# Performance work log

Measured on AMD Instinct MI355X. Metric: run time of the kernel, lower is better.

Reference implementation:

```python
import jax, jax.numpy as jnp
import numpy as np

B, N, H, V = 2048, 16, 512, 780  # trees, nodes per tree, hidden size, vocab size


def _topology():
    """Build one random tree, replicate across B trees, and precompute the
    BFS level schedule on the non-backtracking line graph (as DGL's
    level_order: reversed(edges_back) = up edges leaves-first, then
    edges = down edges root-first)."""
    rng = np.random.default_rng(0)
    parent = np.zeros(N, dtype=np.int64)
    for i in range(1, N):
        parent[i] = rng.integers(0, i)
    depth = np.zeros(N, dtype=np.int64)
    for i in range(1, N):
        depth[i] = depth[parent[i]] + 1
    Epc = 2 * (N - 1)  # directed edges per tree
    src = np.zeros(Epc, dtype=np.int64)
    dst = np.zeros(Epc, dtype=np.int64)
    for i in range(1, N):
        src[2 * (i - 1)] = parent[i]; dst[2 * (i - 1)] = i          # down edge
        src[2 * (i - 1) + 1] = i;     dst[2 * (i - 1) + 1] = parent[i]  # up edge
    # line-graph predecessors of edge e=(u->v): edges f=(w->u) with w != v
    preds = [[f for f in range(Epc) if dst[f] == src[e] and src[f] != dst[e]]
             for e in range(Epc)]
    P = max(1, max(len(p) for p in preds))
    preds_pad = np.full((Epc, P), -1, dtype=np.int64)
    for e, p in enumerate(preds):
        preds_pad[e, :len(p)] = p
    D = int(depth.max())
    levels = []
    for d in range(D, 0, -1):   # upward pass, deepest level first
        levels.append([2 * (i - 1) + 1 for i in range(1, N) if depth[i] == d])
    for d in range(1, D + 1):   # downward pass, root first
        levels.append([2 * (i - 1) for i in range(1, N) if depth[i] == d])
    E = B * Epc                 # index E is the zero dummy row
    offs = np.arange(B, dtype=np.int64) * Epc
    preds_full = np.where(preds_pad[None] >= 0,
                          preds_pad[None] + offs[:, None, None], E)
    preds_full = preds_full.reshape(E, P)
    preds_full = np.concatenate(
        [preds_full, np.full((1, P), E, dtype=np.int64)], axis=0)  # [E+1, P]
    Mmax = max(len(lv) for lv in levels) * B
    lv_arr = np.full((len(levels), Mmax), E, dtype=np.int64)
    for l, lv in enumerate(levels):
        ids = (np.asarray(lv, np.int64)[None] + offs[:, None]).reshape(-1)
        lv_arr[l, :ids.size] = ids
    edge_src = (src[None] + np.arange(B, dtype=np.int64)[:, None] * N).reshape(-1)
    root_children = [2 * (i - 1) + 1 for i in range(1, N) if parent[i] == 0]
    root_in = np.asarray(root_children, np.int64)[None] + offs[:, None]  # [B, R]
    root_nodes = np.arange(B, dtype=np.int64) * N
    return edge_src, preds_full, lv_arr, root_in, root_nodes


def setup_inputs() -> dict:
    key = jax.random.key(0)
    ks = jax.random.split(key, 11)
    edge_src, preds, levels, root_in, root_nodes = _topology()
    s1 = 1.0 / np.sqrt(H)
    s2 = 1.0 / np.sqrt(2 * H)
    return {
        "wid": jax.random.randint(ks[0], (B * N,), 0, V),
        "edge_src": jnp.asarray(edge_src),
        "preds": jnp.asarray(preds),
        "levels": jnp.asarray(levels),
        "root_in": jnp.asarray(root_in),
        "root_nodes": jnp.asarray(root_nodes),
        "emb": jax.random.normal(ks[1], (V, H), jnp.float32),
        "w_r": jax.random.normal(ks[2], (H, H), jnp.float32) * s1,
        "ur_w": jax.random.normal(ks[3], (H, H), jnp.float32) * s1,
        "ur_b": jax.random.normal(ks[4], (H,), jnp.float32) * s1,
        "wz_w": jax.random.normal(ks[5], (2 * H, H), jnp.float32) * s2,
        "wz_b": jax.random.normal(ks[6], (H,), jnp.float32) * s2,
        "wh_w": jax.random.normal(ks[7], (2 * H, H), jnp.float32) * s2,
        "wh_b": jax.random.normal(ks[8], (H,), jnp.float32) * s2,
        "wo_w": jax.random.normal(ks[9], (2 * H, H), jnp.float32) * s2,
        "wo_b": jax.random.normal(ks[10], (H,), jnp.float32) * s2,
    }


def reference(wid, edge_src, preds, levels, root_in, root_nodes,
              emb, w_r, ur_w, ur_b, wz_w, wz_b, wh_w, wh_b, wo_w, wo_b):
    E = edge_src.shape[0]
    Hd = emb.shape[1]
    x = emb[wid]                                           # [B*N, H]
    zero = jnp.zeros((1, Hd), x.dtype)
    sx_all = x[edge_src]                                   # src_x per edge
    src_x = jnp.concatenate([sx_all, zero], axis=0)        # [E+1, H], row E = 0
    src_x_r = jnp.concatenate([sx_all @ w_r, zero], axis=0)  # W_r (no bias)
    h = jnp.zeros((E + 1, Hd), x.dtype)
    for l in range(levels.shape[0]):                       # static BFS levels
        idx = levels[l]                                    # [M], padded with E
        p = preds[idx]                                     # [M, P]
        h_nei = h[p]                                       # [M, P, H]
        sum_h = h_nei.sum(axis=1)
        # GRUMessage: r = sigmoid(dst.src_x_r + U_r(src.h)); m = r * src.h
        r = jax.nn.sigmoid(src_x_r[idx][:, None, :] + h_nei @ ur_w + ur_b)
        sum_g = (r * h_nei).sum(axis=1)
        sx = src_x[idx]
        # GRUUpdate
        z = jax.nn.sigmoid(jnp.concatenate([sx, sum_h], axis=-1) @ wz_w + wz_b)
        pre_h = jnp.tanh(jnp.concatenate([sx, sum_g], axis=-1) @ wh_w + wh_b)
        h = h.at[idx].set((1.0 - z) * sum_h + z * pre_h)
        h = h.at[E].set(0.0)                               # keep dummy row zero
    h_edges = h[:E]                                        # edata['h']
    h_root = h[root_in].sum(axis=1)                        # pull into roots
    x_root = x[root_nodes]
    root_vec = jax.nn.relu(
        jnp.concatenate([x_root, h_root], axis=-1) @ wo_w + wo_b)
    return h_edges, root_vec
```

## Files before the change

kernel.cpp:

```cpp
#include <hip/hip_runtime.h>
#include <hip/hip_bf16.h>
#include <cstddef>

#define HD 512

typedef short s8v __attribute__((ext_vector_type(8)));
typedef short s4v __attribute__((ext_vector_type(4)));
typedef float fx4 __attribute__((ext_vector_type(4)));

#define MFMA(a, b, c) __builtin_amdgcn_mfma_f32_16x16x32_bf16((a), (b), (c), 0, 0, 0)

__device__ __forceinline__ unsigned short f2bf(float f) {
  unsigned int u = __float_as_uint(f);
  unsigned int r = (u + 0x7fffu + ((u >> 16) & 1u)) >> 16;
  return (unsigned short)r;
}
__device__ __forceinline__ float bf2f(unsigned short u) {
  return __uint_as_float(((unsigned int)u) << 16);
}

__device__ __forceinline__ size_t swz_off(int k, int n, int KT) {
  int kt = k >> 5, kr = k & 31;
  int nt = n >> 4, nr = n & 15;
  int lane = ((kr >> 3) << 4) | nr;
  int i = kr & 7;
  return ((((size_t)nt * KT + kt) * 64 + lane) << 3) + i;
}

__global__ void pack_kernel(const float* w_r, const float* ur, const float* wz, const float* wh,
                            const float* wo,
                            unsigned short* W1, unsigned short* WZB, unsigned short* WHB,
                            unsigned short* WUR, unsigned short* WO) {
  int idx = blockIdx.x * blockDim.x + threadIdx.x;
  int stride = gridDim.x * blockDim.x;
  for (int t = idx; t < 512 * 1536; t += stride) {
    int k = t / 1536, n = t - k * 1536;
    float v;
    if (n < 512) v = w_r[k * 512 + n];
    else if (n < 1024) v = wz[k * 512 + (n - 512)];
    else v = wh[k * 512 + (n - 1024)];
    W1[swz_off(k, n, 16)] = f2bf(v);
  }
  for (int t = idx; t < 512 * 512; t += stride) {
    int k = t >> 9, n = t & 511;
    size_t o = swz_off(k, n, 16);
    WZB[o] = f2bf(wz[(512 + k) * 512 + n]);
    WHB[o] = f2bf(wh[(512 + k) * 512 + n]);
    WUR[o] = f2bf(ur[k * 512 + n]);
  }
  for (int t = idx; t < 1024 * 512; t += stride) {
    int k = t >> 9, n = t & 511;
    WO[swz_off(k, n, 32)] = f2bf(wo[k * 512 + n]);
  }
}

__global__ void embed_kernel(const int* wid, const float* emb, unsigned short* x_bf, int BN) {
  int idx = blockIdx.x * blockDim.x + threadIdx.x;
  int stride = gridDim.x * blockDim.x;
  int total = BN * (HD / 8);
  for (int t = idx; t < total; t += stride) {
    int nrow = t >> 6;
    int c8 = (t & 63) << 3;
    int w = wid[nrow];
    const float4* s = (const float4*)(emb + (size_t)w * HD + c8);
    float4 v0 = s[0], v1 = s[1];
    s8v o;
    o[0] = (short)f2bf(v0.x); o[1] = (short)f2bf(v0.y);
    o[2] = (short)f2bf(v0.z); o[3] = (short)f2bf(v0.w);
    o[4] = (short)f2bf(v1.x); o[5] = (short)f2bf(v1.y);
    o[6] = (short)f2bf(v1.z); o[7] = (short)f2bf(v1.w);
    *(s8v*)&x_bf[(size_t)nrow * HD + c8] = o;
  }
}

__global__ void schedule_kernel(const int* preds, int E, int Epc, int P, int* sched) {
  __shared__ int rnd[64];
  int t = threadIdx.x;
  rnd[t] = -1;
  __syncthreads();
  for (int it = 0; it <= Epc; ++it) {
    int newv = -1;
    if (t < Epc && rnd[t] < 0) {
      int mx = 0;
      bool ready = true;
      for (int q = 0; q < P; ++q) {
        int pe = preds[t * P + q];
        if (pe < E) {
          int rp = rnd[pe];
          if (rp < 0) ready = false;
          else if (rp + 1 > mx) mx = rp + 1;
        }
      }
      if (ready) newv = mx;
    }
    __syncthreads();
    if (newv >= 0) rnd[t] = newv;
    __syncthreads();
  }
  if (t == 0) {
    int R = 0;
    for (int e = 0; e < Epc; ++e) if (rnd[e] + 1 > R) R = rnd[e] + 1;
    if (R > 31) R = 31;
    sched[0] = R;
    for (int r = 0; r < 31; ++r) {
      int c = 0;
      if (r < R) {
        for (int e = 0; e < Epc; ++e) if (rnd[e] == r) { sched[33 + r * 32 + c] = e; ++c; }
      }
      sched[1 + r] = c;
    }
  }
}

__global__ __launch_bounds__(512, 4) void gemm_pre_kernel(const unsigned short* x_bf,
                                                          const unsigned short* W1,
                                                          unsigned short* XP, int BN) {
  __shared__ unsigned short lA[2][128 * 72];
  const int nM = BN >> 7;
  const int slab = blockIdx.x / nM;
  const int mt = blockIdx.x - slab * nM;
  const int tid = threadIdx.x, lane = tid & 63, w = tid >> 6;
  const int wm = w & 1, wn = w >> 1;
  const int m0 = mt << 7;
  const int srow = tid >> 2, sc0 = (tid & 3) << 4;
  const int k8 = (lane >> 4) << 3;
  fx4 ac[16];
#pragma unroll
  for (int i = 0; i < 16; i++) { ac[i][0]=0.f; ac[i][1]=0.f; ac[i][2]=0.f; ac[i][3]=0.f; }
  const unsigned short* aptr = x_bf + (size_t)(m0 + srow) * 512 + sc0;
  s8v r0, r1;
  {
    r0 = *(const s8v*)aptr;
    r1 = *(const s8v*)(aptr + 8);
    *(s8v*)&lA[0][srow * 72 + sc0]     = r0;
    *(s8v*)&lA[0][srow * 72 + sc0 + 8] = r1;
    r0 = *(const s8v*)(aptr + 64);
    r1 = *(const s8v*)(aptr + 72);
  }
  for (int ks = 0; ks < 8; ++ks) {
    const int cur = ks & 1;
    __syncthreads();
    if (ks < 7) {
      *(s8v*)&lA[cur ^ 1][srow * 72 + sc0]     = r0;
      *(s8v*)&lA[cur ^ 1][srow * 72 + sc0 + 8] = r1;
    }
    if (ks < 6) {
      const unsigned short* g = aptr + ((ks + 2) << 6);
      r0 = *(const s8v*)g;
      r1 = *(const s8v*)(g + 8);
    }
#pragma unroll
    for (int sub = 0; sub < 2; ++sub) {
      const int kt = (ks << 1) + sub;
      s8v a[4];
#pragma unroll
      for (int mi = 0; mi < 4; ++mi)
        a[mi] = *(const s8v*)&lA[cur][((wm << 6) + (mi << 4) + (lane & 15)) * 72 + (sub << 5) + k8];
#pragma unroll
      for (int ni = 0; ni < 4; ++ni) {
        const int ntile = (slab << 4) + (wn << 2) + ni;
        const s8v b = *(const s8v*)(W1 + ((((size_t)ntile << 4) + kt) * 64 + lane) * 8);
#pragma unroll
        for (int mi = 0; mi < 4; ++mi) ac[mi * 4 + ni] = MFMA(a[mi], b, ac[mi * 4 + ni]);
      }
    }
  }
#pragma unroll
  for (int mi = 0; mi < 4; ++mi) {
#pragma unroll
    for (int q = 0; q < 4; ++q) {
      const int row = (wm << 6) + (mi << 4) + ((lane >> 4) << 2) + q;
#pragma unroll
      for (int ni = 0; ni < 4; ++ni) {
        const int col = (slab << 8) + (wn << 6) + (ni << 4) + (lane & 15);
        XP[(size_t)(m0 + row) * 1536 + col] = f2bf(ac[mi * 4 + ni][q]);
      }
    }
  }
}

struct AP {
  const int* sched;
  const int* preds;
  const int* edge_src;
  const float* ur_b;
  const unsigned short* XP;
  const unsigned short* u_bf_c;
  const unsigned short* hE_c;
  unsigned short* A2h;
  unsigned short* A2g;
  int* eIdx;
  int* srcIdx;
  int B, Epc, P, E;
};

__global__ __launch_bounds__(256) void gatherA_kernel(AP p, int r) {
  const int cnt = p.sched[1 + r];
  if (cnt == 0) return;
  const int M = cnt * p.B;
  const int* lst = p.sched + 33 + r * 32;
  const int lane = threadIdx.x & 63;
  const int waveId = blockIdx.x * 4 + (threadIdx.x >> 6);
  const int totalWaves = gridDim.x * 4;
  for (int m = waveId; m < M; m += totalWaves) {
    const int b = m / cnt;
    const int j = m - b * cnt;
    const int e = b * p.Epc + lst[j];
    const int src = p.edge_src[e];
    if (lane == 0) { p.eIdx[m] = e; p.srcIdx[m] = src; }
    const int c0 = lane << 3;
    const s8v xr8 = *(const s8v*)&p.XP[(size_t)src * 1536 + c0];
    float xb[8], ub[8], sh[8], sg[8];
#pragma unroll
    for (int i = 0; i < 8; i++) {
      xb[i] = bf2f((unsigned short)xr8[i]);
      ub[i] = p.ur_b[c0 + i];
      sh[i] = 0.f; sg[i] = 0.f;
    }
    for (int t = 0; t < p.P; ++t) {
      const int pe = p.preds[(size_t)e * p.P + t];
      if (pe >= p.E) continue;
      const s8v h8 = *(const s8v*)&p.hE_c[(size_t)pe * 512 + c0];
      const s8v u8 = *(const s8v*)&p.u_bf_c[(size_t)pe * 512 + c0];
#pragma unroll
      for (int i = 0; i < 8; i++) {
        const float hv = bf2f((unsigned short)h8[i]);
        const float rr = 1.f / (1.f + __expf(-(xb[i] + bf2f((unsigned short)u8[i]) + ub[i])));
        sh[i] += hv;
        sg[i] += rr * hv;
      }
    }
    s8v shb, sgb;
#pragma unroll
    for (int i = 0; i < 8; i++) { shb[i] = (short)f2bf(sh[i]); sgb[i] = (short)f2bf(sg[i]); }
    *(s8v*)&p.A2h[(size_t)m * 512 + c0] = shb;
    *(s8v*)&p.A2g[(size_t)m * 512 + c0] = sgb;
  }
}

struct BP {
  const int* sched;
  const float* wz_b;
  const float* wh_b;
  const unsigned short* XP;
  const unsigned short* A2h;
  const unsigned short* A2g;
  const unsigned short* WZB;
  const unsigned short* WHB;
  const int* eIdx;
  const int* srcIdx;
  unsigned short* hE;
  int B;
};

__global__ __launch_bounds__(256, 4) void gemmB_kernel(BP p, int r) {
  const int cnt = p.sched[1 + r];
  if (cnt == 0) return;
  const int M = cnt * p.B;
  const int nT = (M >> 5) << 1;
  const int qq = nT >> 3;
  __shared__ unsigned short lZ[2][32 * 72];
  __shared__ unsigned short lH[2][32 * 72];
  __shared__ int eL[32];
  __shared__ int sL[32];
  const int tid = threadIdx.x, lane = tid & 63, w = tid >> 6;
  const int srow = tid >> 3, sc = (tid & 7) << 3;
  const int k8 = (lane >> 4) << 3;

  for (int t0 = blockIdx.x; t0 < nT; t0 += gridDim.x) {
    const int t = (t0 & 7) * qq + (t0 >> 3);
    const int mt = t >> 1, nb = t & 1;
    const int m0 = mt << 5, n0 = nb << 8;
    if (tid < 32) { eL[tid] = p.eIdx[m0 + tid]; sL[tid] = p.srcIdx[m0 + tid]; }
    fx4 aZ[8], aH[8];
#pragma unroll
    for (int i = 0; i < 8; i++) {
      aZ[i][0]=0.f; aZ[i][1]=0.f; aZ[i][2]=0.f; aZ[i][3]=0.f;
      aH[i][0]=0.f; aH[i][1]=0.f; aH[i][2]=0.f; aH[i][3]=0.f;
    }
    const size_t rbase = (size_t)(m0 + srow) * 512 + sc;
    s8v nh, ng;
    {
      *(s8v*)&lZ[0][srow * 72 + sc] = *(const s8v*)&p.A2h[rbase];
      *(s8v*)&lH[0][srow * 72 + sc] = *(const s8v*)&p.A2g[rbase];
      nh = *(const s8v*)&p.A2h[rbase + 64];
      ng = *(const s8v*)&p.A2g[rbase + 64];
    }
    for (int ks = 0; ks < 8; ++ks) {
      const int cur = ks & 1;
      __syncthreads();
      if (ks < 7) {
        *(s8v*)&lZ[cur ^ 1][srow * 72 + sc] = nh;
        *(s8v*)&lH[cur ^ 1][srow * 72 + sc] = ng;
      }
      if (ks < 6) {
        nh = *(const s8v*)&p.A2h[rbase + ((ks + 2) << 6)];
        ng = *(const s8v*)&p.A2g[rbase + ((ks + 2) << 6)];
      }
#pragma unroll
      for (int sub = 0; sub < 2; ++sub) {
        const int kt = (ks << 1) + sub;
        s8v az[2], ah[2];
#pragma unroll
        for (int mi = 0; mi < 2; ++mi) {
          const int ao = ((mi << 4) + (lane & 15)) * 72 + (sub << 5) + k8;
          az[mi] = *(const s8v*)&lZ[cur][ao];
          ah[mi] = *(const s8v*)&lH[cur][ao];
        }
#pragma unroll
        for (int ni = 0; ni < 4; ++ni) {
          const int ntile = (n0 >> 4) + (w << 2) + ni;
          const size_t boff = ((((size_t)ntile << 4) + kt) * 64 + lane) << 3;
          const s8v bz = *(const s8v*)(p.WZB + boff);
          const s8v bh = *(const s8v*)(p.WHB + boff);
#pragma unroll
          for (int mi = 0; mi < 2; ++mi) {
            aZ[mi * 4 + ni] = MFMA(az[mi], bz, aZ[mi * 4 + ni]);
            aH[mi * 4 + ni] = MFMA(ah[mi], bh, aH[mi * 4 + ni]);
          }
        }
      }
    }
#pragma unroll
    for (int mi = 0; mi < 2; ++mi) {
#pragma unroll
      for (int q4 = 0; q4 < 4; ++q4) {
        const int row = (mi << 4) + ((lane >> 4) << 2) + q4;
        const int e = eL[row];
        const int src = sL[row];
#pragma unroll
        for (int ni = 0; ni < 4; ++ni) {
          const int col = n0 + (w << 6) + (ni << 4) + (lane & 15);
          float zpre = aZ[mi * 4 + ni][q4] + bf2f(p.XP[(size_t)src * 1536 + 512 + col]) + p.wz_b[col];
          float hpre = aH[mi * 4 + ni][q4] + bf2f(p.XP[(size_t)src * 1536 + 1024 + col]) + p.wh_b[col];
          float zz = 1.f / (1.f + __expf(-zpre));
          float e2 = __expf(2.f * hpre);
          float th = 1.f - 2.f / (e2 + 1.f);
          float sumh = bf2f(p.A2h[(size_t)(m0 + row) * 512 + col]);
          float hn = (1.f - zz) * sumh + zz * th;
          p.hE[(size_t)e * 512 + col] = f2bf(hn);
        }
      }
    }
    __syncthreads();
  }
}

struct CP {
  const int* sched;
  const unsigned short* hE;
  const unsigned short* WUR;
  const int* eIdx;
  unsigned short* u_bf;
  int B;
};

__global__ __launch_bounds__(256, 4) void gemmC_kernel(CP p, int r) {
  const int cnt = p.sched[1 + r];
  if (cnt == 0) return;
  const int M = cnt * p.B;
  const int nT = (M >> 5) << 1;
  const int qq = nT >> 3;
  __shared__ unsigned short lA[2][32 * 72];
  __shared__ int eL[32];
  const int tid = threadIdx.x, lane = tid & 63, w = tid >> 6;
  const int srow = tid >> 3, sc = (tid & 7) << 3;
  const int k8 = (lane >> 4) << 3;

  for (int t0 = blockIdx.x; t0 < nT; t0 += gridDim.x) {
    const int t = (t0 & 7) * qq + (t0 >> 3);
    const int mt = t >> 1, nb = t & 1;
    const int m0 = mt << 5, n0 = nb << 8;
    if (tid < 32) eL[tid] = p.eIdx[m0 + tid];
    __syncthreads();
    fx4 ac[8];
#pragma unroll
    for (int i = 0; i < 8; i++) { ac[i][0]=0.f; ac[i][1]=0.f; ac[i][2]=0.f; ac[i][3]=0.f; }
    const unsigned short* gbase = p.hE + (size_t)eL[srow] * 512 + sc;
    s8v ra;
    {
      *(s8v*)&lA[0][srow * 72 + sc] = *(const s8v*)gbase;
      ra = *(const s8v*)(gbase + 64);
    }
    for (int ks = 0; ks < 8; ++ks) {
      const int cur = ks & 1;
      __syncthreads();
      if (ks < 7) {
        *(s8v*)&lA[cur ^ 1][srow * 72 + sc] = ra;
      }
      if (ks < 6) {
        ra = *(const s8v*)(gbase + ((ks + 2) << 6));
      }
#pragma unroll
      for (int sub = 0; sub < 2; ++sub) {
        const int kt = (ks << 1) + sub;
        s8v a[2];
#pragma unroll
        for (int mi = 0; mi < 2; ++mi)
          a[mi] = *(const s8v*)&lA[cur][((mi << 4) + (lane & 15)) * 72 + (sub << 5) + k8];
#pragma unroll
        for (int ni = 0; ni < 4; ++ni) {
          const int ntile = (n0 >> 4) + (w << 2) + ni;
          const size_t boff = ((((size_t)ntile << 4) + kt) * 64 + lane) << 3;
          const s8v bu = *(const s8v*)(p.WUR + boff);
#pragma unroll
          for (int mi = 0; mi < 2; ++mi) ac[mi * 4 + ni] = MFMA(a[mi], bu, ac[mi * 4 + ni]);
        }
      }
    }
#pragma unroll
    for (int mi = 0; mi < 2; ++mi) {
#pragma unroll
      for (int q4 = 0; q4 < 4; ++q4) {
        const int row = (mi << 4) + ((lane >> 4) << 2) + q4;
        const int e = eL[row];
#pragma unroll
        for (int ni = 0; ni < 4; ++ni) {
          const int col = n0 + (w << 6) + (ni << 4) + (lane & 15);
          p.u_bf[(size_t)e * 512 + col] = f2bf(ac[mi * 4 + ni][q4]);
        }
      }
    }
    __syncthreads();
  }
}

__global__ void cvt_kernel(const unsigned short* hE, float* h, int total8) {
  int idx = blockIdx.x * blockDim.x + threadIdx.x;
  int stride = gridDim.x * blockDim.x;
  for (int t = idx; t < total8; t += stride) {
    const s8v v = *(const s8v*)&hE[(size_t)t * 8];
    float4 f0 = make_float4(bf2f((unsigned short)v[0]), bf2f((unsigned short)v[1]),
                            bf2f((unsigned short)v[2]), bf2f((unsigned short)v[3]));
    float4 f1 = make_float4(bf2f((unsigned short)v[4]), bf2f((unsigned short)v[5]),
                            bf2f((unsigned short)v[6]), bf2f((unsigned short)v[7]));
    *(float4*)&h[(size_t)t * 8] = f0;
    *(float4*)&h[(size_t)t * 8 + 4] = f1;
  }
}

__global__ void root_gather_kernel(const int* root_nodes, const int* root_in,
                                   const unsigned short* x_bf, const unsigned short* hE,
                                   unsigned short* Aroot, int B, int R0) {
  int lane = threadIdx.x & 63;
  int waveId = blockIdx.x * (blockDim.x >> 6) + (threadIdx.x >> 6);
  int totalWaves = gridDim.x * (blockDim.x >> 6);
  for (int b = waveId; b < B; b += totalWaves) {
    int c0 = lane << 3;
    int nd = root_nodes[b];
    *(s8v*)&Aroot[(size_t)b * 1024 + c0] = *(const s8v*)&x_bf[(size_t)nd * HD + c0];
    float s[8];
#pragma unroll
    for (int i = 0; i < 8; i++) s[i] = 0.f;
    for (int t = 0; t < R0; ++t) {
      int e = root_in[b * R0 + t];
      const s8v h8 = *(const s8v*)&hE[(size_t)e * 512 + c0];
#pragma unroll
      for (int i = 0; i < 8; i++) s[i] += bf2f((unsigned short)h8[i]);
    }
    s8v sb;
#pragma unroll
    for (int i = 0; i < 8; i++) sb[i] = (short)f2bf(s[i]);
    *(s8v*)&Aroot[(size_t)b * 1024 + 512 + c0] = sb;
  }
}

__global__ __launch_bounds__(256, 4) void gemm_root_kernel(const unsigned short* Aroot,
                                                           const unsigned short* WO,
                                                           const float* wo_b, float* out, int B) {
  const int nT = (B >> 5) << 1;
  __shared__ unsigned short lA[2][32 * 72];
  const int tid = threadIdx.x, lane = tid & 63, w = tid >> 6;
  const int srow = tid >> 3, sc = (tid & 7) << 3;
  const int k8 = (lane >> 4) << 3;

  for (int t = blockIdx.x; t < nT; t += gridDim.x) {
    const int mt = t >> 1, nb = t & 1;
    const int m0 = mt << 5, n0 = nb << 8;
    fx4 ac[8];
#pragma unroll
    for (int i = 0; i < 8; i++) { ac[i][0]=0.f; ac[i][1]=0.f; ac[i][2]=0.f; ac[i][3]=0.f; }
    const unsigned short* gbase = Aroot + (size_t)(m0 + srow) * 1024 + sc;
    s8v ra;
    {
      *(s8v*)&lA[0][srow * 72 + sc] = *(const s8v*)gbase;
      ra = *(const s8v*)(gbase + 64);
    }
    for (int ks = 0; ks < 16; ++ks) {
      const int cur = ks & 1;
      __syncthreads();
      if (ks < 15) {
        *(s8v*)&lA[cur ^ 1][srow * 72 + sc] = ra;
      }
      if (ks < 14) {
        ra = *(const s8v*)(gbase + ((ks + 2) << 6));
      }
#pragma unroll
      for (int sub = 0; sub < 2; ++sub) {
        const int kt = (ks << 1) + sub;
        s8v a[2];
#pragma unroll
        for (int mi = 0; mi < 2; ++mi)
          a[mi] = *(const s8v*)&lA[cur][((mi << 4) + (lane & 15)) * 72 + (sub << 5) + k8];
#pragma unroll
        for (int ni = 0; ni < 4; ++ni) {
          const int ntile = (n0 >> 4) + (w << 2) + ni;
          const size_t boff = (((size_t)ntile * 32 + kt) * 64 + lane) << 3;
          const s8v b = *(const s8v*)(WO + boff);
#pragma unroll
          for (int mi = 0; mi < 2; ++mi) ac[mi * 4 + ni] = MFMA(a[mi], b, ac[mi * 4 + ni]);
        }
      }
    }
#pragma unroll
    for (int mi = 0; mi < 2; ++mi) {
#pragma unroll
      for (int q4 = 0; q4 < 4; ++q4) {
        const int row = (mi << 4) + ((lane >> 4) << 2) + q4;
        const int m = m0 + row;
#pragma unroll
        for (int ni = 0; ni < 4; ++ni) {
          const int col = n0 + (w << 6) + (ni << 4) + (lane & 15);
          float v = ac[mi * 4 + ni][q4] + wo_b[col];
          out[(size_t)m * HD + col] = v > 0.f ? v : 0.f;
        }
      }
    }
    __syncthreads();
  }
}

extern "C" void kernel_launch(void* const* d_in, const int* in_sizes, int n_in,
                              void* d_out, int out_size, void* d_ws, size_t ws_size,
                              hipStream_t stream) {
  const int* wid = (const int*)d_in[0];
  const int* edge_src = (const int*)d_in[1];
  const int* preds = (const int*)d_in[2];
  const int* root_in = (const int*)d_in[4];
  const int* root_nodes = (const int*)d_in[5];
  const float* emb = (const float*)d_in[6];
  const float* w_r = (const float*)d_in[7];
  const float* ur_w = (const float*)d_in[8];
  const float* ur_b = (const float*)d_in[9];
  const float* wz_w = (const float*)d_in[10];
  const float* wz_b = (const float*)d_in[11];
  const float* wh_w = (const float*)d_in[12];
  const float* wh_b = (const float*)d_in[13];
  const float* wo_w = (const float*)d_in[14];
  const float* wo_b = (const float*)d_in[15];

  const int BN = in_sizes[0];
  const int E = in_sizes[1];
  const int Bt = in_sizes[5];
  const int Epc = E / Bt;
  const int P = in_sizes[2] / (E + 1);
  const int R0 = in_sizes[4] / Bt;

  float* h = (float*)d_out;

  char* wp = (char*)d_ws;
  auto alloc = [&](size_t bytes) {
    char* r = wp;
    wp += (bytes + 255) & ~(size_t)255;
    return r;
  };
  unsigned short* x_bf = (unsigned short*)alloc((size_t)BN * 512 * 2);
  unsigned short* XP = (unsigned short*)alloc((size_t)BN * 1536 * 2);
  unsigned short* u_bf = (unsigned short*)alloc((size_t)E * 512 * 2);
  unsigned short* hE = (unsigned short*)alloc((size_t)E * 512 * 2);
  unsigned short* A2h = (unsigned short*)alloc((size_t)E * 512 * 2);
  unsigned short* A2g = (unsigned short*)alloc((size_t)E * 512 * 2);
  int* eIdx = (int*)alloc((size_t)E * 4);
  int* srcIdx = (int*)alloc((size_t)E * 4);
  unsigned short* W1 = (unsigned short*)alloc((size_t)512 * 1536 * 2);
  unsigned short* WZB = (unsigned short*)alloc((size_t)512 * 512 * 2);
  unsigned short* WHB = (unsigned short*)alloc((size_t)512 * 512 * 2);
  unsigned short* WUR = (unsigned short*)alloc((size_t)512 * 512 * 2);
  unsigned short* WO = (unsigned short*)alloc((size_t)1024 * 512 * 2);
  unsigned short* Aroot = (unsigned short*)alloc((size_t)Bt * 1024 * 2);
  int* sched = (int*)alloc(8192);

  hipLaunchKernelGGL(pack_kernel, dim3(512), dim3(256), 0, stream,
                     w_r, ur_w, wz_w, wh_w, wo_w, W1, WZB, WHB, WUR, WO);
  hipLaunchKernelGGL(embed_kernel, dim3(1024), dim3(256), 0, stream, wid, emb, x_bf, BN);
  hipLaunchKernelGGL(schedule_kernel, dim3(1), dim3(64), 0, stream, preds, E, Epc, P, sched);
  hipLaunchKernelGGL(gemm_pre_kernel, dim3((BN / 128) * 6), dim3(512), 0, stream,
                     x_bf, W1, XP, BN);

  AP ap;
  ap.sched = sched; ap.preds = preds; ap.edge_src = edge_src;
  ap.ur_b = ur_b; ap.XP = XP; ap.u_bf_c = u_bf; ap.hE_c = hE;
  ap.A2h = A2h; ap.A2g = A2g; ap.eIdx = eIdx; ap.srcIdx = srcIdx;
  ap.B = Bt; ap.Epc = Epc; ap.P = P; ap.E = E;

  BP bp;
  bp.sched = sched; bp.wz_b = wz_b; bp.wh_b = wh_b;
  bp.XP = XP; bp.A2h = A2h; bp.A2g = A2g;
  bp.WZB = WZB; bp.WHB = WHB;
  bp.eIdx = eIdx; bp.srcIdx = srcIdx;
  bp.hE = hE; bp.B = Bt;

  CP cp;
  cp.sched = sched; cp.hE = hE; cp.WUR = WUR;
  cp.eIdx = eIdx; cp.u_bf = u_bf; cp.B = Bt;

  for (int r = 0; r < Epc && r < 31; ++r) {
    const int g = (r < 16) ? 1024 : 128;
    hipLaunchKernelGGL(gatherA_kernel, dim3(g), dim3(256), 0, stream, ap, r);
    hipLaunchKernelGGL(gemmB_kernel, dim3(g), dim3(256), 0, stream, bp, r);
    hipLaunchKernelGGL(gemmC_kernel, dim3(g), dim3(256), 0, stream, cp, r);
  }

  hipLaunchKernelGGL(cvt_kernel, dim3(2048), dim3(256), 0, stream, hE, h, E * 64);
  hipLaunchKernelGGL(root_gather_kernel, dim3(512), dim3(256), 0, stream,
                     root_nodes, root_in, x_bf, hE, Aroot, Bt, R0);
  hipLaunchKernelGGL(gemm_root_kernel, dim3((Bt / 32) * 2), dim3(256), 0, stream,
                     Aroot, WO, wo_b, h + (size_t)E * 512, Bt);
}
```

Baseline: 944.7 us.

## Interleave h and U_r(h) rows into one buffer, chunk gather loop, shrink late grids

```diff
diff --git a/kernel.cpp b/kernel.cpp
--- a/kernel.cpp
+++ b/kernel.cpp
@@ -185,8 +185,7 @@
   const int* edge_src;
   const float* ur_b;
   const unsigned short* XP;
-  const unsigned short* u_bf_c;
-  const unsigned short* hE_c;
+  const unsigned short* hu_c;
   unsigned short* A2h;
   unsigned short* A2g;
   int* eIdx;
@@ -202,7 +201,10 @@
   const int lane = threadIdx.x & 63;
   const int waveId = blockIdx.x * 4 + (threadIdx.x >> 6);
   const int totalWaves = gridDim.x * 4;
-  for (int m = waveId; m < M; m += totalWaves) {
+  const int chunk = (M + totalWaves - 1) / totalWaves;
+  const int mBeg = waveId * chunk;
+  const int mEnd = (mBeg + chunk < M) ? (mBeg + chunk) : M;
+  for (int m = mBeg; m < mEnd; ++m) {
     const int b = m / cnt;
     const int j = m - b * cnt;
     const int e = b * p.Epc + lst[j];
@@ -220,8 +222,9 @@
     for (int t = 0; t < p.P; ++t) {
       const int pe = p.preds[(size_t)e * p.P + t];
       if (pe >= p.E) continue;
-      const s8v h8 = *(const s8v*)&p.hE_c[(size_t)pe * 512 + c0];
-      const s8v u8 = *(const s8v*)&p.u_bf_c[(size_t)pe * 512 + c0];
+      const unsigned short* hurow = p.hu_c + (size_t)pe * 1024;
+      const s8v h8 = *(const s8v*)&hurow[c0];
+      const s8v u8 = *(const s8v*)&hurow[512 + c0];
 #pragma unroll
       for (int i = 0; i < 8; i++) {
         const float hv = bf2f((unsigned short)h8[i]);
@@ -249,7 +252,7 @@
   const unsigned short* WHB;
   const int* eIdx;
   const int* srcIdx;
-  unsigned short* hE;
+  unsigned short* hu;
   int B;
 };
 
@@ -338,7 +341,7 @@
           float th = 1.f - 2.f / (e2 + 1.f);
           float sumh = bf2f(p.A2h[(size_t)(m0 + row) * 512 + col]);
           float hn = (1.f - zz) * sumh + zz * th;
-          p.hE[(size_t)e * 512 + col] = f2bf(hn);
+          p.hu[(size_t)e * 1024 + col] = f2bf(hn);
         }
       }
     }
@@ -348,10 +351,9 @@
 
 struct CP {
   const int* sched;
-  const unsigned short* hE;
   const unsigned short* WUR;
   const int* eIdx;
-  unsigned short* u_bf;
+  unsigned short* hu;
   int B;
 };
 
@@ -376,7 +378,7 @@
     fx4 ac[8];
 #pragma unroll
     for (int i = 0; i < 8; i++) { ac[i][0]=0.f; ac[i][1]=0.f; ac[i][2]=0.f; ac[i][3]=0.f; }
-    const unsigned short* gbase = p.hE + (size_t)eL[srow] * 512 + sc;
+    const unsigned short* gbase = p.hu + (size_t)eL[srow] * 1024 + sc;
     s8v ra;
     {
       *(s8v*)&lA[0][srow * 72 + sc] = *(const s8v*)gbase;
@@ -417,7 +419,7 @@
 #pragma unroll
         for (int ni = 0; ni < 4; ++ni) {
           const int col = n0 + (w << 6) + (ni << 4) + (lane & 15);
-          p.u_bf[(size_t)e * 512 + col] = f2bf(ac[mi * 4 + ni][q4]);
+          p.hu[(size_t)e * 1024 + 512 + col] = f2bf(ac[mi * 4 + ni][q4]);
         }
       }
     }
@@ -425,22 +427,24 @@
   }
 }
 
-__global__ void cvt_kernel(const unsigned short* hE, float* h, int total8) {
+__global__ void cvt_kernel(const unsigned short* hu, float* h, int total8) {
   int idx = blockIdx.x * blockDim.x + threadIdx.x;
   int stride = gridDim.x * blockDim.x;
   for (int t = idx; t < total8; t += stride) {
-    const s8v v = *(const s8v*)&hE[(size_t)t * 8];
+    const int row = t >> 6;
+    const int c8 = (t & 63) << 3;
+    const s8v v = *(const s8v*)&hu[(size_t)row * 1024 + c8];
     float4 f0 = make_float4(bf2f((unsigned short)v[0]), bf2f((unsigned short)v[1]),
                             bf2f((unsigned short)v[2]), bf2f((unsigned short)v[3]));
     float4 f1 = make_float4(bf2f((unsigned short)v[4]), bf2f((unsigned short)v[5]),
                             bf2f((unsigned short)v[6]), bf2f((unsigned short)v[7]));
-    *(float4*)&h[(size_t)t * 8] = f0;
-    *(float4*)&h[(size_t)t * 8 + 4] = f1;
+    *(float4*)&h[(size_t)row * 512 + c8] = f0;
+    *(float4*)&h[(size_t)row * 512 + c8 + 4] = f1;
   }
 }
 
 __global__ void root_gather_kernel(const int* root_nodes, const int* root_in,
-                                   const unsigned short* x_bf, const unsigned short* hE,
+                                   const unsigned short* x_bf, const unsigned short* hu,
                                    unsigned short* Aroot, int B, int R0) {
   int lane = threadIdx.x & 63;
   int waveId = blockIdx.x * (blockDim.x >> 6) + (threadIdx.x >> 6);
@@ -454,7 +458,7 @@
     for (int i = 0; i < 8; i++) s[i] = 0.f;
     for (int t = 0; t < R0; ++t) {
       int e = root_in[b * R0 + t];
-      const s8v h8 = *(const s8v*)&hE[(size_t)e * 512 + c0];
+      const s8v h8 = *(const s8v*)&hu[(size_t)e * 1024 + c0];
 #pragma unroll
       for (int i = 0; i < 8; i++) s[i] += bf2f((unsigned short)h8[i]);
     }
@@ -566,8 +570,7 @@
   };
   unsigned short* x_bf = (unsigned short*)alloc((size_t)BN * 512 * 2);
   unsigned short* XP = (unsigned short*)alloc((size_t)BN * 1536 * 2);
-  unsigned short* u_bf = (unsigned short*)alloc((size_t)E * 512 * 2);
-  unsigned short* hE = (unsigned short*)alloc((size_t)E * 512 * 2);
+  unsigned short* hu = (unsigned short*)alloc((size_t)E * 1024 * 2);
   unsigned short* A2h = (unsigned short*)alloc((size_t)E * 512 * 2);
   unsigned short* A2g = (unsigned short*)alloc((size_t)E * 512 * 2);
   int* eIdx = (int*)alloc((size_t)E * 4);
@@ -589,7 +592,7 @@
 
   AP ap;
   ap.sched = sched; ap.preds = preds; ap.edge_src = edge_src;
-  ap.ur_b = ur_b; ap.XP = XP; ap.u_bf_c = u_bf; ap.hE_c = hE;
+  ap.ur_b = ur_b; ap.XP = XP; ap.hu_c = hu;
   ap.A2h = A2h; ap.A2g = A2g; ap.eIdx = eIdx; ap.srcIdx = srcIdx;
   ap.B = Bt; ap.Epc = Epc; ap.P = P; ap.E = E;
 
@@ -598,22 +601,22 @@
   bp.XP = XP; bp.A2h = A2h; bp.A2g = A2g;
   bp.WZB = WZB; bp.WHB = WHB;
   bp.eIdx = eIdx; bp.srcIdx = srcIdx;
-  bp.hE = hE; bp.B = Bt;
+  bp.hu = hu; bp.B = Bt;
 
   CP cp;
-  cp.sched = sched; cp.hE = hE; cp.WUR = WUR;
-  cp.eIdx = eIdx; cp.u_bf = u_bf; cp.B = Bt;
+  cp.sched = sched; cp.WUR = WUR;
+  cp.eIdx = eIdx; cp.hu = hu; cp.B = Bt;
 
   for (int r = 0; r < Epc && r < 31; ++r) {
-    const int g = (r < 16) ? 1024 : 128;
+    const int g = (r < 16) ? 1024 : 16;
     hipLaunchKernelGGL(gatherA_kernel, dim3(g), dim3(256), 0, stream, ap, r);
     hipLaunchKernelGGL(gemmB_kernel, dim3(g), dim3(256), 0, stream, bp, r);
     hipLaunchKernelGGL(gemmC_kernel, dim3(g), dim3(256), 0, stream, cp, r);
   }
 
-  hipLaunchKernelGGL(cvt_kernel, dim3(2048), dim3(256), 0, stream, hE, h, E * 64);
+  hipLaunchKernelGGL(cvt_kernel, dim3(2048), dim3(256), 0, stream, hu, h, E * 64);
   hipLaunchKernelGGL(root_gather_kernel, dim3(512), dim3(256), 0, stream,
-                     root_nodes, root_in, x_bf, hE, Aroot, Bt, R0);
+                     root_nodes, root_in, x_bf, hu, Aroot, Bt, R0);
   hipLaunchKernelGGL(gemm_root_kernel, dim3((Bt / 32) * 2), dim3(256), 0, stream,
                      Aroot, WO, wo_b, h + (size_t)E * 512, Bt);
 }
```

After: 950.1 us. About the same (+0.6%).
